# Kernel optimization log

Measured on AMD Instinct MI355X. Metric: run time of the kernel, lower is better.

The kernel has to match this reference:

```python
import jax, jax.numpy as jnp
import numpy as np
from jax import lax

K = 8  # window / output_stride (hardcoded in original forward)
BN_EPS = 1e-5


def setup_inputs() -> dict:
    key = jax.random.key(0)
    ks = jax.random.split(key, 4)
    B, C, H, W = 4, 56, 320, 320
    return {
        "x": jax.random.normal(ks[0], (B, C, H, W), jnp.float32),
        "conv1_w": jax.random.normal(ks[1], (56, 56), jnp.float32) * 0.01,
        "conv1_b": jnp.zeros((56,), jnp.float32),
        "conv2_w": jax.random.normal(ks[2], (1, 56), jnp.float32) * 0.01,
        "conv2_b": jnp.zeros((1,), jnp.float32),
        "bn1_gamma": jnp.ones((56,), jnp.float32),
        "bn1_beta": jnp.zeros((56,), jnp.float32),
        "bn2_gamma": jnp.ones((1,), jnp.float32),
        "bn2_beta": jnp.zeros((1,), jnp.float32),
    }


def _batchnorm(y, gamma, beta):
    # training-mode BatchNorm2d: stats over (N, H, W) per channel
    mean = jnp.mean(y, axis=(0, 2, 3), keepdims=True)
    var = jnp.var(y, axis=(0, 2, 3), keepdims=True)
    yhat = (y - mean) * lax.rsqrt(var + BN_EPS)
    return yhat * gamma[None, :, None, None] + beta[None, :, None, None]


def _counter(x, w1, b1, w2, b2, g1, be1, g2, be2):
    # AvgPool2d(kernel=8, stride=1) -> [B,56,H-7,W-7]
    p = lax.reduce_window(x, 0.0, lax.add, (1, 1, K, K), (1, 1, 1, 1), "VALID") / (K * K)
    y = jnp.einsum("oc,bchw->bohw", w1, p) + b1[None, :, None, None]
    y = jax.nn.relu(_batchnorm(y, g1, be1))
    y = jnp.einsum("oc,bchw->bohw", w2, y) + b2[None, :, None, None]
    y = jax.nn.relu(_batchnorm(y, g2, be2))
    return y  # [B,1,Hc,Wc]


def _dynamic_unfolding(x, local_count):
    # x: [B,C,H,W], local_count: [B,1,H-7,W-7]
    B, C, H, W = x.shape
    Hc, Wc = H - K + 1, W - K + 1
    m = jnp.mean(x, axis=1)  # [B,H,W]
    # extract all 8x8 sliding windows -> [B,Hc,Wc,64]
    patches = jnp.stack(
        [m[:, di:di + Hc, dj:dj + Wc] for di in range(K) for dj in range(K)],
        axis=-1,
    )
    sm = jax.nn.softmax(patches, axis=-1)  # per-window softmax
    wgt = sm * local_count[:, 0, :, :, None]  # [B,Hc,Wc,64]
    # overlapping fold (scatter-add) back to [B,1,H,W]
    R = jnp.zeros((B, H, W), x.dtype)
    for di in range(K):
        for dj in range(K):
            R = R.at[:, di:di + Hc, dj:dj + Wc].add(wgt[..., di * K + dj])
    return R[:, None, :, :]


def reference(x, conv1_w, conv1_b, conv2_w, conv2_b, bn1_gamma, bn1_beta, bn2_gamma, bn2_beta):
    C_out = _counter(x, conv1_w, conv1_b, conv2_w, conv2_b, bn1_gamma, bn1_beta, bn2_gamma, bn2_beta)
    R = _dynamic_unfolding(x, C_out)
    return C_out, R
```

## Files before the change

### kernel.cpp

```cpp
#include <hip/hip_runtime.h>
#include <math.h>

#define B 4
#define C 56
#define H 320
#define W 320
#define HC 313
#define WC 313
#define NIMG (H*W)
#define NSP  (HC*WC)
#define NPIX (B*NSP)
#define NM   (B*NIMG)
#define BN_EPS 1e-5f
#define NGRID 512

#define PHR 39
#define NF4 390

typedef __attribute__((ext_vector_type(8))) short short8;
typedef __attribute__((ext_vector_type(16))) float float16;
typedef __attribute__((ext_vector_type(4))) float f32x4;

__device__ __forceinline__ unsigned short f2bf(float v) {
  unsigned int u = __float_as_uint(v);
  return (unsigned short)((u + 0x7fffu + ((u >> 16) & 1u)) >> 16);
}

__global__ __launch_bounds__(256) void pool32_kernel(
    const float* __restrict__ x, float* __restrict__ Epart,
    unsigned short* __restrict__ p_t) {
  __shared__ float tin[PHR][40];
  __shared__ float hs[PHR][32];
  __shared__ unsigned short Pt[8][1024];
  const int tid = threadIdx.x;
  int bid = blockIdx.x;
  const int g = bid % 7; bid /= 7;
  const int b = bid & 3; bid >>= 2;
  const int ty = bid / 10, tx = bid - (bid / 10) * 10;
  const int i0 = ty * 32, j0 = tx * 32;
  const float* xg = x + ((size_t)b * C + g * 8) * NIMG;

  int r4[2], q4[2]; bool act[2], vld[2], inter[2]; size_t xoff[2];
  #pragma unroll
  for (int k = 0; k < 2; ++k) {
    int idx = tid + k * 256;
    r4[k] = idx / 10; q4[k] = idx - r4[k] * 10;
    act[k] = idx < NF4;
    vld[k] = act[k] && (i0 + r4[k] < H) && (j0 + q4[k] * 4 < W);
    inter[k] = act[k] && r4[k] < 32 && q4[k] < 8;
    xoff[k] = (size_t)(i0 + r4[k]) * W + j0 + q4[k] * 4;
  }
  f32x4 cur4[2], nxt4[2];
  #pragma unroll
  for (int k = 0; k < 2; ++k)
    cur4[k] = vld[k] ? *(const f32x4*)(xg + xoff[k]) : (f32x4){0.f, 0.f, 0.f, 0.f};

  f32x4 esum4[2] = {{0.f, 0.f, 0.f, 0.f}, {0.f, 0.f, 0.f, 0.f}};

  #pragma unroll
  for (int c = 0; c < 8; ++c) {
    #pragma unroll
    for (int k = 0; k < 2; ++k) {
      if (act[k]) *(f32x4*)&tin[r4[k]][q4[k] * 4] = cur4[k];
      if (inter[k]) esum4[k] += cur4[k];
    }
    __syncthreads();
    if (c < 7) {
      const float* xp = xg + (size_t)(c + 1) * NIMG;
      #pragma unroll
      for (int k = 0; k < 2; ++k)
        nxt4[k] = vld[k] ? *(const f32x4*)(xp + xoff[k]) : (f32x4){0.f, 0.f, 0.f, 0.f};
    }
    #pragma unroll
    for (int it = 0; it < 5; ++it) {
      int idx = tid + it * 256;
      if (idx < PHR * 32) {
        int r = idx >> 5, j = idx & 31;
        float s = 0.f;
        #pragma unroll
        for (int d = 0; d < 8; ++d) s += tin[r][j + d];
        hs[r][j] = s;
      }
    }
    __syncthreads();
    #pragma unroll
    for (int it = 0; it < 4; ++it) {
      int idx = tid + it * 256;
      int i = idx >> 5, j = idx & 31;
      float s = 0.f;
      #pragma unroll
      for (int d = 0; d < 8; ++d) s += hs[i + d][j];
      Pt[c][idx] = f2bf(s * (1.f / 64.f));
    }
    #pragma unroll
    for (int k = 0; k < 2; ++k) cur4[k] = nxt4[k];
  }
  __syncthreads();

  float* Eb = Epart + ((size_t)g * B + b) * NIMG;
  #pragma unroll
  for (int k = 0; k < 2; ++k)
    if (inter[k]) *(f32x4*)&Eb[(i0 + r4[k]) * W + j0 + q4[k] * 4] = esum4[k];

  unsigned short* pg = p_t + (size_t)g * NPIX * 8;
  #pragma unroll
  for (int k = 0; k < 4; ++k) {
    int idx = tid + k * 256;
    int i = idx >> 5, j = idx & 31;
    int gi = i0 + i, gj = j0 + j;
    if (gi < HC && gj < WC) {
      unsigned short t8[8];
      #pragma unroll
      for (int c2 = 0; c2 < 8; ++c2) t8[c2] = Pt[c2][idx];
      *(short8*)(pg + ((size_t)b * NSP + gi * WC + gj) * 8) = *(short8*)t8;
    }
  }
}

__global__ __launch_bounds__(256) void se_pool_kernel(
    const float* __restrict__ Epart, float* __restrict__ E, float* __restrict__ S) {
  __shared__ float tin[39][40];
  __shared__ float hs[39][33];
  const int b = blockIdx.z;
  const int i0 = blockIdx.y * 32, j0 = blockIdx.x * 32;
  const int tid = threadIdx.x;
  for (int idx = tid; idx < 39 * 39; idx += 256) {
    int r = idx / 39, cc = idx - r * 39;
    int gi = i0 + r, gj = j0 + cc;
    float v = 0.f;
    if (gi < H && gj < W) {
      float s = 0.f;
      #pragma unroll
      for (int g = 0; g < 7; ++g)
        s += Epart[((size_t)g * B + b) * NIMG + gi * W + gj];
      v = expf(s * (1.f / C));
      if (r < 32 && cc < 32) E[(size_t)b * NIMG + gi * W + gj] = v;
    }
    tin[r][cc] = v;
  }
  __syncthreads();
  for (int idx = tid; idx < 39 * 32; idx += 256) {
    int r = idx >> 5, j = idx & 31;
    float s = 0.f;
    #pragma unroll
    for (int d = 0; d < 8; ++d) s += tin[r][j + d];
    hs[r][j] = s;
  }
  __syncthreads();
  for (int idx = tid; idx < 32 * 32; idx += 256) {
    int i = idx >> 5, j = idx & 31;
    int gi = i0 + i, gj = j0 + j;
    if (gi < HC && gj < WC) {
      float s = 0.f;
      #pragma unroll
      for (int d = 0; d < 8; ++d) s += hs[i + d][j];
      S[(size_t)b * NSP + gi * WC + gj] = s;
    }
  }
}

__global__ __launch_bounds__(256) void y1_stats_kernel(
    const unsigned short* __restrict__ p_t, const float* __restrict__ w1,
    float* __restrict__ ypart) {
  __shared__ unsigned short Wl[64 * 64];
  __shared__ float red[4][32][64];
  const int tid = threadIdx.x, wave = tid >> 6, lane = tid & 63;
  for (int idx = tid; idx < 4096; idx += 256) {
    int o = idx >> 6, k = idx & 63;
    float v = (o < C && k < C) ? w1[o * C + k] : 0.f;
    *(unsigned short*)((char*)Wl + (o * 128 + ((2 * k) ^ ((o & 7) << 4)))) = f2bf(v);
  }
  __syncthreads();
  short8 afr[2][4];
  #pragma unroll
  for (int q = 0; q < 2; ++q)
    #pragma unroll
    for (int ks = 0; ks < 4; ++ks) {
      int row = q * 32 + (lane & 31), kb = ks * 16 + 8 * (lane >> 5);
      afr[q][ks] = *(const short8*)((const char*)Wl + row * 128 + ((2 * kb) ^ ((row & 7) << 4)));
    }
  float s1[2][16], s2[2][16];
  #pragma unroll
  for (int q = 0; q < 2; ++q)
    #pragma unroll
    for (int r = 0; r < 16; ++r) { s1[q][r] = 0.f; s2[q][r] = 0.f; }

  const int h = lane >> 5;
  const int nchunk = (NPIX + 127) / 128;
  for (int ch = blockIdx.x; ch < nchunk; ch += NGRID) {
    int col = ch * 128 + wave * 32 + (lane & 31);
    bool cv = col < NPIX;
    size_t pofs = (size_t)(cv ? col : 0) * 8;
    short8 bfr[4];
    #pragma unroll
    for (int ks = 0; ks < 4; ++ks) {
      int g = ks * 2 + h;
      short8 bv = (short8){0, 0, 0, 0, 0, 0, 0, 0};
      if (g < 7 && cv) bv = *(const short8*)(p_t + (size_t)g * NPIX * 8 + pofs);
      bfr[ks] = bv;
    }
    float16 a0 = {}, a1 = {};
    #pragma unroll
    for (int ks = 0; ks < 4; ++ks) {
      a0 = __builtin_amdgcn_mfma_f32_32x32x16_bf16(afr[0][ks], bfr[ks], a0, 0, 0, 0);
      a1 = __builtin_amdgcn_mfma_f32_32x32x16_bf16(afr[1][ks], bfr[ks], a1, 0, 0, 0);
    }
    #pragma unroll
    for (int r = 0; r < 16; ++r) {
      s1[0][r] += a0[r]; s2[0][r] = fmaf(a0[r], a0[r], s2[0][r]);
      s1[1][r] += a1[r]; s2[1][r] = fmaf(a1[r], a1[r], s2[1][r]);
    }
  }
  for (int pass = 0; pass < 2; ++pass) {
    __syncthreads();
    #pragma unroll
    for (int q = 0; q < 2; ++q)
      #pragma unroll
      for (int r = 0; r < 16; ++r)
        red[wave][q * 16 + r][lane] = pass ? s2[q][r] : s1[q][r];
    __syncthreads();
    if (tid < C) {
      int row = tid, q = row >> 5, rr = row & 31;
      int hh = (rr >> 2) & 1, reg = (rr & 3) | ((rr >> 3) << 2);
      float s = 0.f;
      #pragma unroll
      for (int w = 0; w < 4; ++w)
        #pragma unroll
        for (int cl = 0; cl < 32; ++cl)
          s += red[w][q * 16 + reg][32 * hh + cl];
      ypart[blockIdx.x * 112 + pass * 56 + row] = s;
    }
  }
}

__global__ void ypart_bn1_kernel(const float* __restrict__ ypart,
                                 const float* __restrict__ g1, const float* __restrict__ be1,
                                 float* __restrict__ ac) {
  __shared__ float sums[112];
  int t = threadIdx.x;
  if (t < 112) {
    float s0 = 0.f, s1 = 0.f, s2 = 0.f, s3 = 0.f;
    #pragma unroll 4
    for (int b = 0; b < NGRID; b += 4) {
      s0 += ypart[(b + 0) * 112 + t];
      s1 += ypart[(b + 1) * 112 + t];
      s2 += ypart[(b + 2) * 112 + t];
      s3 += ypart[(b + 3) * 112 + t];
    }
    sums[t] = (s0 + s1) + (s2 + s3);
  }
  __syncthreads();
  if (t < C) {
    float m = sums[t] * (1.f / NPIX);
    float var = sums[56 + t] * (1.f / NPIX) - m * m;
    float a = g1[t] * rsqrtf(var + BN_EPS);
    ac[t] = a;
    ac[C + t] = fmaf(-a, m, be1[t]);
  }
}

__global__ __launch_bounds__(256) void y2_kernel(
    const unsigned short* __restrict__ p_t, const float* __restrict__ w1,
    const float* __restrict__ ac, const float* __restrict__ w2,
    float* __restrict__ y2, float* __restrict__ stats2) {
  __shared__ unsigned short Wl[64 * 64];
  __shared__ float af[64], cf[64], wf[64];
  const int tid = threadIdx.x, wave = tid >> 6, lane = tid & 63;
  for (int idx = tid; idx < 4096; idx += 256) {
    int o = idx >> 6, k = idx & 63;
    float v = (o < C && k < C) ? w1[o * C + k] : 0.f;
    *(unsigned short*)((char*)Wl + (o * 128 + ((2 * k) ^ ((o & 7) << 4)))) = f2bf(v);
  }
  if (tid < 64) {
    bool ok = tid < C;
    af[tid] = ok ? ac[tid] : 0.f;
    cf[tid] = ok ? ac[C + tid] : 0.f;
    wf[tid] = ok ? w2[tid] : 0.f;
  }
  __syncthreads();
  short8 afr[2][4];
  #pragma unroll
  for (int q = 0; q < 2; ++q)
    #pragma unroll
    for (int ks = 0; ks < 4; ++ks) {
      int row = q * 32 + (lane & 31), kb = ks * 16 + 8 * (lane >> 5);
      afr[q][ks] = *(const short8*)((const char*)Wl + row * 128 + ((2 * kb) ^ ((row & 7) << 4)));
    }
  const int h = lane >> 5;
  float ss1 = 0.f, ss2 = 0.f;
  const int nchunk = (NPIX + 127) / 128;
  for (int ch = blockIdx.x; ch < nchunk; ch += NGRID) {
    int col = ch * 128 + wave * 32 + (lane & 31);
    bool cv = col < NPIX;
    size_t pofs = (size_t)(cv ? col : 0) * 8;
    short8 bfr[4];
    #pragma unroll
    for (int ks = 0; ks < 4; ++ks) {
      int g = ks * 2 + h;
      short8 bv = (short8){0, 0, 0, 0, 0, 0, 0, 0};
      if (g < 7 && cv) bv = *(const short8*)(p_t + (size_t)g * NPIX * 8 + pofs);
      bfr[ks] = bv;
    }
    float16 a0 = {}, a1 = {};
    #pragma unroll
    for (int ks = 0; ks < 4; ++ks) {
      a0 = __builtin_amdgcn_mfma_f32_32x32x16_bf16(afr[0][ks], bfr[ks], a0, 0, 0, 0);
      a1 = __builtin_amdgcn_mfma_f32_32x32x16_bf16(afr[1][ks], bfr[ks], a1, 0, 0, 0);
    }
    float ysum = 0.f;
    #pragma unroll
    for (int r = 0; r < 16; ++r) {
      int o0 = (r & 3) + 8 * (r >> 2) + 4 * h;
      ysum = fmaf(wf[o0], fmaxf(fmaf(af[o0], a0[r], cf[o0]), 0.f), ysum);
      int o1 = o0 + 32;
      ysum = fmaf(wf[o1], fmaxf(fmaf(af[o1], a1[r], cf[o1]), 0.f), ysum);
    }
    ysum += __shfl_xor(ysum, 32);
    bool wr = cv && lane < 32;
    if (wr) {
      y2[col] = ysum;
      ss1 += ysum;
      ss2 = fmaf(ysum, ysum, ss2);
    }
  }
  #pragma unroll
  for (int off = 1; off < 64; off <<= 1) {
    ss1 += __shfl_xor(ss1, off);
    ss2 += __shfl_xor(ss2, off);
  }
  if (lane == 0) {
    atomicAdd(&stats2[(blockIdx.x & 63) * 2 + 0], ss1);
    atomicAdd(&stats2[(blockIdx.x & 63) * 2 + 1], ss2);
  }
}

__global__ void bn2_final_kernel(const float* __restrict__ stats2,
                                 const float* __restrict__ g2, const float* __restrict__ be2,
                                 float* __restrict__ a2c2) {
  int t = threadIdx.x;
  float s1 = stats2[t * 2], s2 = stats2[t * 2 + 1];
  #pragma unroll
  for (int off = 32; off > 0; off >>= 1) {
    s1 += __shfl_down(s1, off);
    s2 += __shfl_down(s2, off);
  }
  if (t == 0) {
    float mean = s1 * (1.f / NPIX);
    float var  = s2 * (1.f / NPIX) - mean * mean;
    float a = g2[0] * rsqrtf(var + BN_EPS);
    a2c2[0] = a;
    a2c2[1] = fmaf(-a, mean, be2[0]);
  }
}

__global__ __launch_bounds__(256) void r_pool_kernel(
    const float* __restrict__ y2, const float* __restrict__ S,
    const float* __restrict__ a2c2, const float* __restrict__ E,
    float* __restrict__ cout, float* __restrict__ R) {
  __shared__ float tin[39][40];
  __shared__ float hs[39][33];
  const int b = blockIdx.z;
  const int i0 = blockIdx.y * 32, j0 = blockIdx.x * 32;
  const int tid = threadIdx.x;
  const float a2 = a2c2[0], c2 = a2c2[1];
  const float* y2b = y2 + (size_t)b * NSP;
  const float* Sb  = S + (size_t)b * NSP;
  float* cb = cout + (size_t)b * NSP;
  for (int idx = tid; idx < 39 * 39; idx += 256) {
    int r = idx / 39, cc = idx - r * 39;
    int gi = i0 + r - 7, gj = j0 + cc - 7;
    float t = 0.f;
    if (gi >= 0 && gi < HC && gj >= 0 && gj < WC) {
      float v = fmaxf(fmaf(a2, y2b[gi * WC + gj], c2), 0.f);
      t = v / Sb[gi * WC + gj];
      if (r >= 7 && cc >= 7) cb[gi * WC + gj] = v;
    }
    tin[r][cc] = t;
  }
  __syncthreads();
  for (int idx = tid; idx < 39 * 32; idx += 256) {
    int r = idx >> 5, j = idx & 31;
    float s = 0.f;
    #pragma unroll
    for (int d = 0; d < 8; ++d) s += tin[r][j + d];
    hs[r][j] = s;
  }
  __syncthreads();
  for (int idx = tid; idx < 32 * 32; idx += 256) {
    int i = idx >> 5, j = idx & 31;
    size_t gofs = (size_t)b * NIMG + (i0 + i) * W + (j0 + j);
    float s = 0.f;
    #pragma unroll
    for (int d = 0; d < 8; ++d) s += hs[i + d][j];
    R[gofs] = E[gofs] * s;
  }
}

extern "C" void kernel_launch(void* const* d_in, const int* in_sizes, int n_in,
                              void* d_out, int out_size, void* d_ws, size_t ws_size,
                              hipStream_t stream) {
  const float* x   = (const float*)d_in[0];
  const float* w1  = (const float*)d_in[1];
  const float* w2  = (const float*)d_in[3];
  const float* g1  = (const float*)d_in[5];
  const float* be1 = (const float*)d_in[6];
  const float* g2  = (const float*)d_in[7];
  const float* be2 = (const float*)d_in[8];

  float* out_c = (float*)d_out;
  float* out_r = out_c + NPIX;

  unsigned short* p_t = (unsigned short*)d_ws;
  float* fbase = (float*)(p_t + (size_t)7 * NPIX * 8);
  size_t off = 0;
  float* Epart  = fbase + off; off += (size_t)7 * NM;
  float* E      = fbase + off; off += NM;
  float* Sarr   = fbase + off; off += NPIX;
  float* y2     = fbase + off; off += NPIX;
  float* ypart  = fbase + off; off += (size_t)NGRID * 112;
  float* stats2 = fbase + off; off += 128;
  float* ac     = fbase + off; off += 112;
  float* a2c2   = fbase + off; off += 2;

  hipMemsetAsync(stats2, 0, 128 * sizeof(float), stream);

  pool32_kernel<<<100 * B * 7, 256, 0, stream>>>(x, Epart, p_t);

  dim3 sg(10, 10, B);
  se_pool_kernel<<<sg, 256, 0, stream>>>(Epart, E, Sarr);

  y1_stats_kernel<<<NGRID, 256, 0, stream>>>(p_t, w1, ypart);
  ypart_bn1_kernel<<<1, 128, 0, stream>>>(ypart, g1, be1, ac);
  y2_kernel<<<NGRID, 256, 0, stream>>>(p_t, w1, ac, w2, y2, stats2);
  bn2_final_kernel<<<1, 64, 0, stream>>>(stats2, g2, be2, a2c2);

  dim3 rg(10, 10, B);
  r_pool_kernel<<<rg, 256, 0, stream>>>(y2, Sarr, a2c2, E, out_c, out_r);
}
```

Baseline: 118.2 us.

## Vectorize box-filter sums, prefetch MFMA operands, replace atomics with per-wave partials

The pool kernel's horizontal and vertical 8-tap box sums now use float4 shared-memory loads. The horizontal pass uses a sliding-window update instead of eight scalar adds per output. The y1_stats and y2 kernels software-prefetch the next chunk's bf16 operands into registers before running the current chunk's MFMAs, to hide global-load latency. The BN2 statistics move from atomics plus a memset to per-wave partials reduced by a 256-thread final kernel, which removes one API call and the atomic traffic. The cost is higher register pressure from the prefetch and a small change in float summation order.

```diff
diff --git a/kernel.cpp b/kernel.cpp
--- a/kernel.cpp
+++ b/kernel.cpp
@@ -20,6 +20,7 @@
 typedef __attribute__((ext_vector_type(8))) short short8;
 typedef __attribute__((ext_vector_type(16))) float float16;
 typedef __attribute__((ext_vector_type(4))) float f32x4;
+typedef __attribute__((ext_vector_type(4))) unsigned short u16x4;
 
 __device__ __forceinline__ unsigned short f2bf(float v) {
   unsigned int u = __float_as_uint(v);
@@ -30,7 +31,7 @@
     const float* __restrict__ x, float* __restrict__ Epart,
     unsigned short* __restrict__ p_t) {
   __shared__ float tin[PHR][40];
-  __shared__ float hs[PHR][32];
+  __shared__ float hs[PHR][40];
   __shared__ unsigned short Pt[8][1024];
   const int tid = threadIdx.x;
   int bid = blockIdx.x;
@@ -57,6 +58,11 @@
 
   f32x4 esum4[2] = {{0.f, 0.f, 0.f, 0.f}, {0.f, 0.f, 0.f, 0.f}};
 
+  const int hr = tid >> 3, hg = (tid & 7) * 4;
+  const int hr2 = (tid + 256) >> 3;
+  const bool h2 = tid < (PHR * 8 - 256);
+  const int vi = tid >> 3, vg = (tid & 7) * 4;
+
   #pragma unroll
   for (int c = 0; c < 8; ++c) {
     #pragma unroll
@@ -71,26 +77,35 @@
       for (int k = 0; k < 2; ++k)
         nxt4[k] = vld[k] ? *(const f32x4*)(xp + xoff[k]) : (f32x4){0.f, 0.f, 0.f, 0.f};
     }
-    #pragma unroll
-    for (int it = 0; it < 5; ++it) {
-      int idx = tid + it * 256;
-      if (idx < PHR * 32) {
-        int r = idx >> 5, j = idx & 31;
-        float s = 0.f;
-        #pragma unroll
-        for (int d = 0; d < 8; ++d) s += tin[r][j + d];
-        hs[r][j] = s;
+    {
+      f32x4 a  = *(const f32x4*)&tin[hr][hg];
+      f32x4 bv = *(const f32x4*)&tin[hr][hg + 4];
+      f32x4 cv = *(const f32x4*)&tin[hr][hg + 8];
+      float s0 = ((a[0] + a[1]) + (a[2] + a[3])) + ((bv[0] + bv[1]) + (bv[2] + bv[3]));
+      float s1 = s0 - a[0] + cv[0];
+      float s2 = s1 - a[1] + cv[1];
+      float s3 = s2 - a[2] + cv[2];
+      *(f32x4*)&hs[hr][hg] = (f32x4){s0, s1, s2, s3};
+      if (h2) {
+        f32x4 a2  = *(const f32x4*)&tin[hr2][hg];
+        f32x4 b2  = *(const f32x4*)&tin[hr2][hg + 4];
+        f32x4 c2  = *(const f32x4*)&tin[hr2][hg + 8];
+        float t0 = ((a2[0] + a2[1]) + (a2[2] + a2[3])) + ((b2[0] + b2[1]) + (b2[2] + b2[3]));
+        float t1 = t0 - a2[0] + c2[0];
+        float t2 = t1 - a2[1] + c2[1];
+        float t3 = t2 - a2[2] + c2[2];
+        *(f32x4*)&hs[hr2][hg] = (f32x4){t0, t1, t2, t3};
       }
     }
     __syncthreads();
-    #pragma unroll
-    for (int it = 0; it < 4; ++it) {
-      int idx = tid + it * 256;
-      int i = idx >> 5, j = idx & 31;
-      float s = 0.f;
-      #pragma unroll
-      for (int d = 0; d < 8; ++d) s += hs[i + d][j];
-      Pt[c][idx] = f2bf(s * (1.f / 64.f));
+    {
+      f32x4 s = *(const f32x4*)&hs[vi][vg];
+      #pragma unroll
+      for (int d = 1; d < 8; ++d) s += *(const f32x4*)&hs[vi + d][vg];
+      u16x4 o;
+      #pragma unroll
+      for (int k = 0; k < 4; ++k) o[k] = f2bf(s[k] * (1.f / 64.f));
+      *(u16x4*)&Pt[c][vi * 32 + vg] = o;
     }
     #pragma unroll
     for (int k = 0; k < 2; ++k) cur4[k] = nxt4[k];
@@ -187,18 +202,23 @@
 
   const int h = lane >> 5;
   const int nchunk = (NPIX + 127) / 128;
+  auto loadch = [&](int cc, short8* dst) {
+    int col = cc * 128 + wave * 32 + (lane & 31);
+    bool cv = (cc < nchunk) && (col < NPIX);
+    size_t pofs = (size_t)(cv ? col : 0) * 8;
+    #pragma unroll
+    for (int ks = 0; ks < 4; ++ks) {
+      int gg = ks * 2 + h;
+      short8 bv = (short8){0, 0, 0, 0, 0, 0, 0, 0};
+      if (gg < 7 && cv) bv = *(const short8*)(p_t + (size_t)gg * NPIX * 8 + pofs);
+      dst[ks] = bv;
+    }
+  };
+  short8 bfr[4];
+  loadch(blockIdx.x, bfr);
   for (int ch = blockIdx.x; ch < nchunk; ch += NGRID) {
-    int col = ch * 128 + wave * 32 + (lane & 31);
-    bool cv = col < NPIX;
-    size_t pofs = (size_t)(cv ? col : 0) * 8;
-    short8 bfr[4];
-    #pragma unroll
-    for (int ks = 0; ks < 4; ++ks) {
-      int g = ks * 2 + h;
-      short8 bv = (short8){0, 0, 0, 0, 0, 0, 0, 0};
-      if (g < 7 && cv) bv = *(const short8*)(p_t + (size_t)g * NPIX * 8 + pofs);
-      bfr[ks] = bv;
-    }
+    short8 nbfr[4];
+    loadch(ch + NGRID, nbfr);
     float16 a0 = {}, a1 = {};
     #pragma unroll
     for (int ks = 0; ks < 4; ++ks) {
@@ -210,6 +230,8 @@
       s1[0][r] += a0[r]; s2[0][r] = fmaf(a0[r], a0[r], s2[0][r]);
       s1[1][r] += a1[r]; s2[1][r] = fmaf(a1[r], a1[r], s2[1][r]);
     }
+    #pragma unroll
+    for (int ks = 0; ks < 4; ++ks) bfr[ks] = nbfr[ks];
   }
   for (int pass = 0; pass < 2; ++pass) {
     __syncthreads();
@@ -262,7 +284,7 @@
 __global__ __launch_bounds__(256) void y2_kernel(
     const unsigned short* __restrict__ p_t, const float* __restrict__ w1,
     const float* __restrict__ ac, const float* __restrict__ w2,
-    float* __restrict__ y2, float* __restrict__ stats2) {
+    float* __restrict__ y2, float* __restrict__ y2part) {
   __shared__ unsigned short Wl[64 * 64];
   __shared__ float af[64], cf[64], wf[64];
   const int tid = threadIdx.x, wave = tid >> 6, lane = tid & 63;
@@ -289,18 +311,23 @@
   const int h = lane >> 5;
   float ss1 = 0.f, ss2 = 0.f;
   const int nchunk = (NPIX + 127) / 128;
+  auto loadch = [&](int cc, short8* dst) {
+    int col = cc * 128 + wave * 32 + (lane & 31);
+    bool cv = (cc < nchunk) && (col < NPIX);
+    size_t pofs = (size_t)(cv ? col : 0) * 8;
+    #pragma unroll
+    for (int ks = 0; ks < 4; ++ks) {
+      int gg = ks * 2 + h;
+      short8 bv = (short8){0, 0, 0, 0, 0, 0, 0, 0};
+      if (gg < 7 && cv) bv = *(const short8*)(p_t + (size_t)gg * NPIX * 8 + pofs);
+      dst[ks] = bv;
+    }
+  };
+  short8 bfr[4];
+  loadch(blockIdx.x, bfr);
   for (int ch = blockIdx.x; ch < nchunk; ch += NGRID) {
-    int col = ch * 128 + wave * 32 + (lane & 31);
-    bool cv = col < NPIX;
-    size_t pofs = (size_t)(cv ? col : 0) * 8;
-    short8 bfr[4];
-    #pragma unroll
-    for (int ks = 0; ks < 4; ++ks) {
-      int g = ks * 2 + h;
-      short8 bv = (short8){0, 0, 0, 0, 0, 0, 0, 0};
-      if (g < 7 && cv) bv = *(const short8*)(p_t + (size_t)g * NPIX * 8 + pofs);
-      bfr[ks] = bv;
-    }
+    short8 nbfr[4];
+    loadch(ch + NGRID, nbfr);
     float16 a0 = {}, a1 = {};
     #pragma unroll
     for (int ks = 0; ks < 4; ++ks) {
@@ -316,12 +343,15 @@
       ysum = fmaf(wf[o1], fmaxf(fmaf(af[o1], a1[r], cf[o1]), 0.f), ysum);
     }
     ysum += __shfl_xor(ysum, 32);
-    bool wr = cv && lane < 32;
+    int col = ch * 128 + wave * 32 + (lane & 31);
+    bool wr = (col < NPIX) && lane < 32;
     if (wr) {
       y2[col] = ysum;
       ss1 += ysum;
       ss2 = fmaf(ysum, ysum, ss2);
     }
+    #pragma unroll
+    for (int ks = 0; ks < 4; ++ks) bfr[ks] = nbfr[ks];
   }
   #pragma unroll
   for (int off = 1; off < 64; off <<= 1) {
@@ -329,22 +359,32 @@
     ss2 += __shfl_xor(ss2, off);
   }
   if (lane == 0) {
-    atomicAdd(&stats2[(blockIdx.x & 63) * 2 + 0], ss1);
-    atomicAdd(&stats2[(blockIdx.x & 63) * 2 + 1], ss2);
-  }
-}
-
-__global__ void bn2_final_kernel(const float* __restrict__ stats2,
+    y2part[(blockIdx.x * 4 + wave) * 2 + 0] = ss1;
+    y2part[(blockIdx.x * 4 + wave) * 2 + 1] = ss2;
+  }
+}
+
+__global__ void bn2_final_kernel(const float* __restrict__ y2part,
                                  const float* __restrict__ g2, const float* __restrict__ be2,
                                  float* __restrict__ a2c2) {
+  __shared__ float red[8];
   int t = threadIdx.x;
-  float s1 = stats2[t * 2], s2 = stats2[t * 2 + 1];
+  float s1 = 0.f, s2 = 0.f;
+  for (int i = t; i < NGRID * 4; i += 256) {
+    s1 += y2part[i * 2 + 0];
+    s2 += y2part[i * 2 + 1];
+  }
   #pragma unroll
   for (int off = 32; off > 0; off >>= 1) {
     s1 += __shfl_down(s1, off);
     s2 += __shfl_down(s2, off);
   }
+  int wave = t >> 6, lane = t & 63;
+  if (lane == 0) { red[wave * 2] = s1; red[wave * 2 + 1] = s2; }
+  __syncthreads();
   if (t == 0) {
+    s1 = red[0] + red[2] + red[4] + red[6];
+    s2 = red[1] + red[3] + red[5] + red[7];
     float mean = s1 * (1.f / NPIX);
     float var  = s2 * (1.f / NPIX) - mean * mean;
     float a = g2[0] * rsqrtf(var + BN_EPS);
@@ -418,12 +458,10 @@
   float* Sarr   = fbase + off; off += NPIX;
   float* y2     = fbase + off; off += NPIX;
   float* ypart  = fbase + off; off += (size_t)NGRID * 112;
-  float* stats2 = fbase + off; off += 128;
+  float* y2part = fbase + off; off += (size_t)NGRID * 8;
   float* ac     = fbase + off; off += 112;
   float* a2c2   = fbase + off; off += 2;
 
-  hipMemsetAsync(stats2, 0, 128 * sizeof(float), stream);
-
   pool32_kernel<<<100 * B * 7, 256, 0, stream>>>(x, Epart, p_t);
 
   dim3 sg(10, 10, B);
@@ -431,8 +469,8 @@
 
   y1_stats_kernel<<<NGRID, 256, 0, stream>>>(p_t, w1, ypart);
   ypart_bn1_kernel<<<1, 128, 0, stream>>>(ypart, g1, be1, ac);
-  y2_kernel<<<NGRID, 256, 0, stream>>>(p_t, w1, ac, w2, y2, stats2);
-  bn2_final_kernel<<<1, 64, 0, stream>>>(stats2, g2, be2, a2c2);
+  y2_kernel<<<NGRID, 256, 0, stream>>>(p_t, w1, ac, w2, y2, y2part);
+  bn2_final_kernel<<<1, 256, 0, stream>>>(y2part, g2, be2, a2c2);
 
   dim3 rg(10, 10, B);
   r_pool_kernel<<<rg, 256, 0, stream>>>(y2, Sarr, a2c2, E, out_c, out_r);
```

Measured after the change: 104.8 us. 1.13x faster.
